# Kernel optimization log

Hardware: AMD Instinct MI355X
Metric: run time of the kernel (lower is better)

Reference implementation:

```python
import jax, jax.numpy as jnp
import numpy as np

B, T, C, HS = 4, 4096, 1024, 128

def setup_inputs() -> dict:
    key = jax.random.key(0)
    kx, kk, kq, kv = jax.random.split(key, 4)
    x = jax.random.normal(kx, (B, T, C), dtype=jnp.float32)
    # torch Linear(n_embd, head_size, bias=False): y = x @ W.T with W [hs, C].
    # We store the transposed form W [C, hs] so y = x @ W (same math).
    s = C ** -0.5  # kaiming-ish scale to keep activations sane
    Wk = jax.random.normal(kk, (C, HS), dtype=jnp.float32) * s
    Wq = jax.random.normal(kq, (C, HS), dtype=jnp.float32) * s
    Wv = jax.random.normal(kv, (C, HS), dtype=jnp.float32) * s
    return {"x": x, "Wk": Wk, "Wq": Wq, "Wv": Wv}

def reference(x, Wk, Wq, Wv):
    # Single causal self-attention head (dropout = identity, eval mode).
    k = jnp.einsum('btc,ch->bth', x, Wk)  # [B,T,hs]
    q = jnp.einsum('btc,ch->bth', x, Wq)
    v = jnp.einsum('btc,ch->bth', x, Wv)
    scale = k.shape[-1] ** -0.5
    wei = jnp.einsum('bqh,bkh->bqk', q, k) * scale  # [B,T,T]
    Tq = x.shape[1]
    causal = jnp.tril(jnp.ones((Tq, Tq), dtype=bool))
    wei = jnp.where(causal, wei, -jnp.inf)
    wei = jax.nn.softmax(wei, axis=-1)
    out = jnp.einsum('bqk,bkh->bqh', wei, v)  # [B,T,hs]
    return out
```

## Files before the change

kernel.cpp:

```cpp
#include <hip/hip_runtime.h>
#include <hip/hip_bf16.h>
#include <math.h>

#define B_  4
#define T_  4096
#define C_  1024
#define HS_ 128

using bf16x8 = __attribute__((ext_vector_type(8))) __bf16;
using bf16x4 = __attribute__((ext_vector_type(4))) __bf16;
using f32x4  = __attribute__((ext_vector_type(4))) float;

#define MFMA(a, b, c) __builtin_amdgcn_mfma_f32_16x16x32_bf16(a, b, c, 0, 0, 0)

typedef __attribute__((address_space(1))) const float gfloat;
typedef __attribute__((address_space(3))) float lfloat;

__device__ inline float fexp2(float x) {
  float r;
  asm volatile("v_exp_f32 %0, %1\n\ts_nop 0" : "=v"(r) : "v"(x));
  return r;
}


__global__ __launch_bounds__(256) void prep_w_kernel(
    const float* __restrict__ Wk, const float* __restrict__ Wq,
    const float* __restrict__ Wv, __bf16* __restrict__ Wf) {
  const int m  = blockIdx.x >> 4;
  const int k0 = (blockIdx.x & 15) * 64;
  const float* W = (m == 0) ? Wq : ((m == 1) ? Wk : Wv);
  const float scale = (m == 0) ? (0.08838834764831845f * 1.4426950408889634f) : 1.0f;
  __shared__ __bf16 tile[128][72];
  const int t = threadIdx.x;
#pragma unroll
  for (int p = 0; p < 8; ++p) {
    int e  = p * 1024 + t * 4;
    int r  = e >> 7;
    int cc = e & 127;
    float4 w = *reinterpret_cast<const float4*>(&W[(size_t)(k0 + r) * HS_ + cc]);
    tile[cc + 0][r] = (__bf16)(w.x * scale);
    tile[cc + 1][r] = (__bf16)(w.y * scale);
    tile[cc + 2][r] = (__bf16)(w.z * scale);
    tile[cc + 3][r] = (__bf16)(w.w * scale);
  }
  __syncthreads();
#pragma unroll
  for (int p = 0; p < 4; ++p) {
    int e  = p * 2048 + t * 8;
    int n  = e >> 6;
    int kk = e & 63;
    bf16x8 v;
#pragma unroll
    for (int jj = 0; jj < 8; ++jj) v[jj] = tile[n][kk + jj];
    int u  = m * 8 + (n >> 4);
    int ts = (k0 + kk) >> 5;
    int g2 = (kk >> 3) & 3;
    *reinterpret_cast<bf16x8*>(
        &Wf[((size_t)(u * 32 + ts) * 64 + g2 * 16 + (n & 15)) * 8]) = v;
  }
}

__device__ inline bf16x8 cvt8p(float4 u, float4 v) {
  bf16x8 r;
  r[0] = (__bf16)u.x; r[1] = (__bf16)u.y; r[2] = (__bf16)u.z; r[3] = (__bf16)u.w;
  r[4] = (__bf16)v.x; r[5] = (__bf16)v.y; r[6] = (__bf16)v.z; r[7] = (__bf16)v.w;
  return r;
}

__global__ __launch_bounds__(512) void proj_kernel(
    const float* __restrict__ x, const __bf16* __restrict__ Wf,
    __bf16* __restrict__ Qf, __bf16* __restrict__ Kf, __bf16* __restrict__ Vf) {
  __shared__ __align__(16) char lds[57344];
  const int tid = threadIdx.x;
  const int wid = tid >> 6;
  const int l   = tid & 63;
  const int c   = l & 15;
  const int g   = l >> 4;
  const int rbase = blockIdx.x * 32;

  f32x4 acc[3][2];
#pragma unroll
  for (int i = 0; i < 3; ++i) { acc[i][0] = 0.f; acc[i][1] = 0.f; }

  const int xrow = (tid & 255) >> 3;
  const int xch  = tid & 7;
  const float* xsrc = x + (size_t)(rbase + xrow) * C_ + ((xch ^ (xrow & 7)) << 2);
  const __bf16* wsrc[3];
  int wdst[3];
#pragma unroll
  for (int i = 0; i < 3; ++i) {
    int id = i * 512 + tid;
    int u  = id >> 6;
    int ln = id & 63;
    wsrc[i] = Wf + (size_t)u * 32 * 512 + ln * 8;
    wdst[i] = 4096 + id * 16;
  }

  auto stage = [&](int t, int bo) {
    if (tid < 256)
      __builtin_amdgcn_global_load_lds((gfloat*)(xsrc + t * 32),
          (lfloat*)(lds + bo + tid * 16), 16, 0, 0);
#pragma unroll
    for (int i = 0; i < 3; ++i)
      __builtin_amdgcn_global_load_lds((gfloat*)(wsrc[i] + t * 512),
          (lfloat*)(lds + bo + wdst[i]), 16, 0, 0);
  };

  int woffs[3];
#pragma unroll
  for (int i = 0; i < 3; ++i)
    woffs[i] = 4096 + (wid * 3 + i) * 1024 + l * 16;
  int xoffs[2][2];
#pragma unroll
  for (int rt = 0; rt < 2; ++rt) {
    int row = rt * 16 + c;
#pragma unroll
    for (int j = 0; j < 2; ++j)
      xoffs[rt][j] = row * 128 + ((((g << 1) | j) ^ (row & 7)) << 4);
  }

  stage(0, 0);
  asm volatile("s_waitcnt vmcnt(0)" ::: "memory");
  __syncthreads();

  for (int t = 0; t < 32; ++t) {
    const int bo = (t & 1) * 28672;
    if (t + 1 < 32) stage(t + 1, bo ^ 28672);

    bf16x8 wf[3];
#pragma unroll
    for (int i = 0; i < 3; ++i)
      wf[i] = *reinterpret_cast<const bf16x8*>(lds + bo + woffs[i]);
#pragma unroll
    for (int rt = 0; rt < 2; ++rt) {
      float4 lo = *reinterpret_cast<const float4*>(lds + bo + xoffs[rt][0]);
      float4 hi = *reinterpret_cast<const float4*>(lds + bo + xoffs[rt][1]);
      bf16x8 a = cvt8p(lo, hi);
#pragma unroll
      for (int i = 0; i < 3; ++i) acc[i][rt] = MFMA(a, wf[i], acc[i][rt]);
    }

    asm volatile("s_waitcnt vmcnt(0)" ::: "memory");
    __syncthreads();
  }

  const size_t tile = blockIdx.x;
#pragma unroll
  for (int i = 0; i < 3; ++i) {
    const int u = wid * 3 + i;
    const int m = u >> 3, nt = u & 7;
    const int gprime = ((nt & 1) << 1) + (c >> 3);
    const int e = c & 7;
    if (m == 0) {
#pragma unroll
      for (int rt = 0; rt < 2; ++rt)
#pragma unroll
        for (int rr = 0; rr < 4; ++rr)
          Qf[(tile * 8 + rt * 4 + (nt >> 1)) * 512 +
             (gprime * 16 + 4 * g + rr) * 8 + e] = (__bf16)acc[i][rt][rr];
    } else if (m == 1) {
#pragma unroll
      for (int rt = 0; rt < 2; ++rt)
#pragma unroll
        for (int rr = 0; rr < 4; ++rr)
          Kf[(tile * 8 + 2 * (nt >> 1) + (g & 1)) * 512 +
             (gprime * 16 + (((2 * rt + (g >> 1)) << 2) | rr)) * 8 + e] =
              (__bf16)acc[i][rt][rr];
    } else {
#pragma unroll
      for (int rt = 0; rt < 2; ++rt) {
        bf16x4 v4;
#pragma unroll
        for (int rr = 0; rr < 4; ++rr) v4[rr] = (__bf16)acc[i][rt][rr];
        *reinterpret_cast<bf16x4*>(
            Vf + (tile * 8 + nt) * 512 +
            ((2 * rt + (g >> 1)) * 16 + c) * 8 + 4 * (g & 1)) = v4;
      }
    }
  }
}

__global__ __launch_bounds__(256, 2) void attn_kernel(
    const __bf16* __restrict__ Qf, const __bf16* __restrict__ Kf,
    const __bf16* __restrict__ Vf, float* __restrict__ out) {
  __shared__ float sm[4][32];
  __shared__ float sl[4][32];
  __shared__ float bufA[32][132];
  __shared__ float bufB[32][132];

  const int tid = threadIdx.x;
  const int wid = tid >> 6;
  const int l   = tid & 63;
  const int c   = l & 15;
  const int g   = l >> 4;
  const int bid = blockIdx.x;
  const int b   = (bid & 7) >> 1;
  const int j   = ((bid >> 3) << 1) | (bid & 1);
  const int qt  = (j < 64) ? (127 - j) : (j - 64);
  const int qb  = qt * 32;

  bf16x8 qf[2][4];
  {
    const __bf16* Qt = Qf + (size_t)(b * 128 + qt) * 4096 + l * 8;
#pragma unroll
    for (int rt = 0; rt < 2; ++rt)
#pragma unroll
      for (int cs = 0; cs < 4; ++cs)
        qf[rt][cs] = *reinterpret_cast<const bf16x8*>(Qt + (rt * 4 + cs) * 512);
  }

  f32x4 acc[2][8];
#pragma unroll
  for (int i = 0; i < 2; ++i)
#pragma unroll
    for (int d = 0; d < 8; ++d) acc[i][d] = 0.f;
  float mrun[2] = {-INFINITY, -INFINITY};
  float lrun[2] = {0.f, 0.f};

  if (wid <= qt) {
    const __bf16* Kb8 = Kf + (size_t)b * 128 * 4096 + l * 8;
    const __bf16* Vb8 = Vf + (size_t)b * 128 * 4096 + l * 8;
    bf16x8 kreg[8];
    auto kload = [&](int kt) {
      const __bf16* kb = Kb8 + (size_t)kt * 4096;
#pragma unroll
      for (int jj = 0; jj < 8; ++jj)
        kreg[jj] = *reinterpret_cast<const bf16x8*>(kb + jj * 512);
    };
    kload(wid);

    for (int kt = wid; kt <= qt; kt += 4) {
      f32x4 s00 = 0.f, s01 = 0.f, s10 = 0.f, s11 = 0.f;
      __builtin_amdgcn_s_setprio(1);
#pragma unroll
      for (int cs = 0; cs < 4; ++cs) {
        s00 = MFMA(kreg[2 * cs], qf[0][cs], s00);
        s01 = MFMA(kreg[2 * cs + 1], qf[0][cs], s01);
        s10 = MFMA(kreg[2 * cs], qf[1][cs], s10);
        s11 = MFMA(kreg[2 * cs + 1], qf[1][cs], s11);
      }
      __builtin_amdgcn_s_setprio(0);

      bf16x8 vf[8];
      {
        const __bf16* vb = Vb8 + (size_t)kt * 4096;
#pragma unroll
        for (int db = 0; db < 8; ++db)
          vf[db] = *reinterpret_cast<const bf16x8*>(vb + db * 512);
      }

      if (kt + 4 <= qt) kload(kt + 4);

      const bool maskt = (kt == qt);
      bf16x8 pb[2];
#pragma unroll
      for (int rt = 0; rt < 2; ++rt) {
        float p[8];
        const f32x4 sa = rt ? s10 : s00;
        const f32x4 sb = rt ? s11 : s01;
#pragma unroll
        for (int rr = 0; rr < 4; ++rr) { p[rr] = sa[rr]; p[4 + rr] = sb[rr]; }
        if (maskt) {
          const int lim = rt * 16 + c;
#pragma unroll
          for (int jj = 0; jj < 8; ++jj)
            if (8 * g + jj > lim) p[jj] = -INFINITY;
        }
        float t0 = fmaxf(fmaxf(p[0], p[1]), p[2]);
        float t1 = fmaxf(fmaxf(p[3], p[4]), p[5]);
        float t2 = fmaxf(fmaxf(p[6], p[7]), t0);
        float tmax = fmaxf(t1, t2);

        if (!__all(tmax <= mrun[rt] + 11.5415603f)) {
          float cmax = fmaxf(tmax, __shfl_xor(tmax, 16));
          cmax = fmaxf(cmax, __shfl_xor(cmax, 32));
          float mnew = fmaxf(mrun[rt], cmax);
          float al   = fexp2(mrun[rt] - mnew);
          mrun[rt] = mnew;
          lrun[rt] *= al;
#pragma unroll
          for (int db = 0; db < 8; ++db) acc[rt][db] *= al;
        }
        const float mc = mrun[rt];
#pragma unroll
        for (int jj = 0; jj < 8; ++jj) p[jj] = fexp2(p[jj] - mc);
        lrun[rt] += ((p[0] + p[1]) + (p[2] + p[3])) + ((p[4] + p[5]) + (p[6] + p[7]));
#pragma unroll
        for (int jj = 0; jj < 8; ++jj) pb[rt][jj] = (__bf16)p[jj];
      }

      __builtin_amdgcn_s_setprio(1);
#pragma unroll
      for (int db = 0; db < 8; ++db) {
        acc[0][db] = MFMA(vf[db], pb[0], acc[0][db]);
        acc[1][db] = MFMA(vf[db], pb[1], acc[1][db]);
      }
      __builtin_amdgcn_s_setprio(0);
    }
  }

#pragma unroll
  for (int rt = 0; rt < 2; ++rt) {
    lrun[rt] += __shfl_xor(lrun[rt], 16);
    lrun[rt] += __shfl_xor(lrun[rt], 32);
  }

  if (g == 0) {
    sm[wid][c] = mrun[0]; sm[wid][16 + c] = mrun[1];
    sl[wid][c] = lrun[0]; sl[wid][16 + c] = lrun[1];
  }
  __syncthreads();

  float linv[2];
#pragma unroll
  for (int rt = 0; rt < 2; ++rt) {
    const int q = rt * 16 + c;
    float ms = fmaxf(fmaxf(sm[0][q], sm[1][q]), fmaxf(sm[2][q], sm[3][q]));
    float ls = fexp2(sm[0][q] - ms) * sl[0][q] + fexp2(sm[1][q] - ms) * sl[1][q]
             + fexp2(sm[2][q] - ms) * sl[2][q] + fexp2(sm[3][q] - ms) * sl[3][q];
    float al = fexp2(mrun[rt] - ms);
#pragma unroll
    for (int db = 0; db < 8; ++db) acc[rt][db] *= al;
    linv[rt] = 1.0f / ls;
  }

  auto store_buf = [&](float(*buf)[132]) {
#pragma unroll
    for (int rt = 0; rt < 2; ++rt)
#pragma unroll
      for (int db = 0; db < 8; ++db)
        *reinterpret_cast<f32x4*>(&buf[rt * 16 + c][db * 16 + 4 * g]) = acc[rt][db];
  };
  auto add_buf = [&](float(*buf)[132]) {
#pragma unroll
    for (int rt = 0; rt < 2; ++rt)
#pragma unroll
      for (int db = 0; db < 8; ++db)
        acc[rt][db] += *reinterpret_cast<const f32x4*>(&buf[rt * 16 + c][db * 16 + 4 * g]);
  };

  if (wid == 2) store_buf(bufA);
  if (wid == 3) store_buf(bufB);
  __syncthreads();
  if (wid == 0) add_buf(bufA);
  if (wid == 1) add_buf(bufB);
  __syncthreads();
  if (wid == 1) store_buf(bufA);
  __syncthreads();
  if (wid == 0) {
    add_buf(bufA);
    float* op = out + ((size_t)b * T_ + qb) * HS_;
#pragma unroll
    for (int rt = 0; rt < 2; ++rt)
#pragma unroll
      for (int db = 0; db < 8; ++db) {
        f32x4 v = acc[rt][db] * linv[rt];
        *reinterpret_cast<f32x4*>(op + (size_t)(rt * 16 + c) * HS_ + db * 16 + 4 * g) = v;
      }
  }
}

extern "C" void kernel_launch(void* const* d_in, const int* in_sizes, int n_in,
                              void* d_out, int out_size, void* d_ws, size_t ws_size,
                              hipStream_t stream) {
  const float* x  = (const float*)d_in[0];
  const float* Wk = (const float*)d_in[1];
  const float* Wq = (const float*)d_in[2];
  const float* Wv = (const float*)d_in[3];
  float* out = (float*)d_out;

  char* ws = (char*)d_ws;
  __bf16* Wf = (__bf16*)ws;
  __bf16* Qf = (__bf16*)(ws + 786432);
  __bf16* Kf = (__bf16*)(ws + 786432 + 4194304);
  __bf16* Vf = (__bf16*)(ws + 786432 + 8388608);

  prep_w_kernel<<<48, 256, 0, stream>>>(Wk, Wq, Wv, Wf);
  proj_kernel<<<512, 512, 0, stream>>>(x, Wf, Qf, Kf, Vf);
  attn_kernel<<<512, 256, 0, stream>>>(Qf, Kf, Vf, out);
}
```

Baseline: 64.77 us.

## Triple-buffer x tiles in projection kernel with deeper prefetch

Splits the projection kernel's staging into separate x and W buffers. x now gets a three-deep LDS ring prefetched two steps ahead, while W stays double-buffered. The x load moves from 16-byte loads on half the threads to 4-byte loads on all threads, and the waitcnt is relaxed to vmcnt(2) so more loads stay in flight. The goal is to hide global latency for x in the K loop, at the cost of more LDS and smaller-granularity loads.

```diff
diff --git a/kernel.cpp b/kernel.cpp
--- a/kernel.cpp
+++ b/kernel.cpp
@@ -70,7 +70,7 @@
 __global__ __launch_bounds__(512) void proj_kernel(
     const float* __restrict__ x, const __bf16* __restrict__ Wf,
     __bf16* __restrict__ Qf, __bf16* __restrict__ Kf, __bf16* __restrict__ Vf) {
-  __shared__ __align__(16) char lds[57344];
+  __shared__ __align__(16) char lds[61440];
   const int tid = threadIdx.x;
   const int wid = tid >> 6;
   const int l   = tid & 63;
@@ -82,9 +82,15 @@
 #pragma unroll
   for (int i = 0; i < 3; ++i) { acc[i][0] = 0.f; acc[i][1] = 0.f; }
 
-  const int xrow = (tid & 255) >> 3;
-  const int xch  = tid & 7;
-  const float* xsrc = x + (size_t)(rbase + xrow) * C_ + ((xch ^ (xrow & 7)) << 2);
+  const float* xsrc[2];
+#pragma unroll
+  for (int op = 0; op < 2; ++op) {
+    int id  = op * 512 + tid;
+    int row = id >> 5;
+    int w   = id & 31;
+    int sf  = ((((w >> 2) ^ (row & 7)) << 2) | (w & 3));
+    xsrc[op] = x + (size_t)(rbase + row) * C_ + sf;
+  }
   const __bf16* wsrc[3];
   int wdst[3];
 #pragma unroll
@@ -93,23 +99,26 @@
     int u  = id >> 6;
     int ln = id & 63;
     wsrc[i] = Wf + (size_t)u * 32 * 512 + ln * 8;
-    wdst[i] = 4096 + id * 16;
-  }
-
-  auto stage = [&](int t, int bo) {
-    if (tid < 256)
-      __builtin_amdgcn_global_load_lds((gfloat*)(xsrc + t * 32),
-          (lfloat*)(lds + bo + tid * 16), 16, 0, 0);
+    wdst[i] = id * 16;
+  }
+
+  auto xstage = [&](int t, int xbo) {
+#pragma unroll
+    for (int op = 0; op < 2; ++op)
+      __builtin_amdgcn_global_load_lds((gfloat*)(xsrc[op] + t * 32),
+          (lfloat*)(lds + xbo + (op * 512 + tid) * 4), 4, 0, 0);
+  };
+  auto wstage = [&](int t, int wbo) {
 #pragma unroll
     for (int i = 0; i < 3; ++i)
       __builtin_amdgcn_global_load_lds((gfloat*)(wsrc[i] + t * 512),
-          (lfloat*)(lds + bo + wdst[i]), 16, 0, 0);
+          (lfloat*)(lds + wbo + wdst[i]), 16, 0, 0);
   };
 
   int woffs[3];
 #pragma unroll
   for (int i = 0; i < 3; ++i)
-    woffs[i] = 4096 + (wid * 3 + i) * 1024 + l * 16;
+    woffs[i] = (wid * 3 + i) * 1024 + l * 16;
   int xoffs[2][2];
 #pragma unroll
   for (int rt = 0; rt < 2; ++rt) {
@@ -119,29 +128,39 @@
       xoffs[rt][j] = row * 128 + ((((g << 1) | j) ^ (row & 7)) << 4);
   }
 
-  stage(0, 0);
-  asm volatile("s_waitcnt vmcnt(0)" ::: "memory");
-  __syncthreads();
-
+  xstage(0, 0);
+  wstage(0, 12288);
+  xstage(1, 4096);
+  asm volatile("s_waitcnt vmcnt(2)" ::: "memory");
+  __syncthreads();
+
+  int xb_cur = 0, xb_nxt = 4096, xb_fut = 8192;
   for (int t = 0; t < 32; ++t) {
-    const int bo = (t & 1) * 28672;
-    if (t + 1 < 32) stage(t + 1, bo ^ 28672);
+    const int wbo = 12288 + (t & 1) * 24576;
+    if (t + 1 < 32) wstage(t + 1, 12288 + ((t + 1) & 1) * 24576);
+    const bool more2 = (t + 2 < 32);
+    if (more2) xstage(t + 2, xb_fut);
 
     bf16x8 wf[3];
 #pragma unroll
     for (int i = 0; i < 3; ++i)
-      wf[i] = *reinterpret_cast<const bf16x8*>(lds + bo + woffs[i]);
+      wf[i] = *reinterpret_cast<const bf16x8*>(lds + wbo + woffs[i]);
 #pragma unroll
     for (int rt = 0; rt < 2; ++rt) {
-      float4 lo = *reinterpret_cast<const float4*>(lds + bo + xoffs[rt][0]);
-      float4 hi = *reinterpret_cast<const float4*>(lds + bo + xoffs[rt][1]);
+      float4 lo = *reinterpret_cast<const float4*>(lds + xb_cur + xoffs[rt][0]);
+      float4 hi = *reinterpret_cast<const float4*>(lds + xb_cur + xoffs[rt][1]);
       bf16x8 a = cvt8p(lo, hi);
 #pragma unroll
       for (int i = 0; i < 3; ++i) acc[i][rt] = MFMA(a, wf[i], acc[i][rt]);
     }
 
-    asm volatile("s_waitcnt vmcnt(0)" ::: "memory");
+    if (more2) {
+      asm volatile("s_waitcnt vmcnt(2)" ::: "memory");
+    } else {
+      asm volatile("s_waitcnt vmcnt(0)" ::: "memory");
+    }
     __syncthreads();
+    int tmp = xb_cur; xb_cur = xb_nxt; xb_nxt = xb_fut; xb_fut = tmp;
   }
 
   const size_t tile = blockIdx.x;
```

Measured after the change: 65.05 us. No clear change (+0.4%).

## Retile projection GEMM to 128-row blocks per Q/K/V matrix

Applied to the files above, without the earlier changes.

The projection kernel now gives each block 128 rows of x and a single output matrix (Q, K or V), with four waves that each compute 32 rows by 128 columns. Before, a block handled 32 rows across all three weights. The new tiling lowers the weight bytes staged per row of x, since each weight tile is reused over 128 rows. The cost is that x is read three times, once per matrix, and the grid shrinks to 384 blocks of 256 threads with more accumulators per thread.

```diff
diff --git a/kernel.cpp b/kernel.cpp
--- a/kernel.cpp
+++ b/kernel.cpp
@@ -67,53 +67,59 @@
   return r;
 }
 
-__global__ __launch_bounds__(512) void proj_kernel(
+__global__ __launch_bounds__(256) void proj_kernel(
     const float* __restrict__ x, const __bf16* __restrict__ Wf,
     __bf16* __restrict__ Qf, __bf16* __restrict__ Kf, __bf16* __restrict__ Vf) {
-  __shared__ __align__(16) char lds[57344];
+  __shared__ __align__(16) char lds[49152];
   const int tid = threadIdx.x;
   const int wid = tid >> 6;
   const int l   = tid & 63;
   const int c   = l & 15;
   const int g   = l >> 4;
-  const int rbase = blockIdx.x * 32;
-
-  f32x4 acc[3][2];
-#pragma unroll
-  for (int i = 0; i < 3; ++i) { acc[i][0] = 0.f; acc[i][1] = 0.f; }
-
-  const int xrow = (tid & 255) >> 3;
-  const int xch  = tid & 7;
-  const float* xsrc = x + (size_t)(rbase + xrow) * C_ + ((xch ^ (xrow & 7)) << 2);
-  const __bf16* wsrc[3];
-  int wdst[3];
-#pragma unroll
-  for (int i = 0; i < 3; ++i) {
-    int id = i * 512 + tid;
-    int u  = id >> 6;
+  const int m       = blockIdx.x % 3;
+  const int rowtile = blockIdx.x / 3;
+  const int rbase   = rowtile * 128;
+
+  f32x4 acc[8][2];
+#pragma unroll
+  for (int i = 0; i < 8; ++i) { acc[i][0] = 0.f; acc[i][1] = 0.f; }
+
+  const float* xsrc[4];
+#pragma unroll
+  for (int op = 0; op < 4; ++op) {
+    int id  = op * 256 + tid;
+    int row = id >> 3;
+    int ch  = id & 7;
+    xsrc[op] = x + (size_t)(rbase + row) * C_ + ((ch ^ (row & 7)) << 2);
+  }
+  const __bf16* wsrc[2];
+#pragma unroll
+  for (int i = 0; i < 2; ++i) {
+    int id = i * 256 + tid;
+    int ul = id >> 6;
     int ln = id & 63;
-    wsrc[i] = Wf + (size_t)u * 32 * 512 + ln * 8;
-    wdst[i] = 4096 + id * 16;
+    wsrc[i] = Wf + (size_t)((m * 8 + ul) * 32) * 512 + ln * 8;
   }
 
   auto stage = [&](int t, int bo) {
-    if (tid < 256)
-      __builtin_amdgcn_global_load_lds((gfloat*)(xsrc + t * 32),
-          (lfloat*)(lds + bo + tid * 16), 16, 0, 0);
-#pragma unroll
-    for (int i = 0; i < 3; ++i)
+#pragma unroll
+    for (int op = 0; op < 4; ++op)
+      __builtin_amdgcn_global_load_lds((gfloat*)(xsrc[op] + t * 32),
+          (lfloat*)(lds + bo + (op * 256 + tid) * 16), 16, 0, 0);
+#pragma unroll
+    for (int i = 0; i < 2; ++i)
       __builtin_amdgcn_global_load_lds((gfloat*)(wsrc[i] + t * 512),
-          (lfloat*)(lds + bo + wdst[i]), 16, 0, 0);
+          (lfloat*)(lds + bo + 16384 + (i * 256 + tid) * 16), 16, 0, 0);
   };
 
-  int woffs[3];
-#pragma unroll
-  for (int i = 0; i < 3; ++i)
-    woffs[i] = 4096 + (wid * 3 + i) * 1024 + l * 16;
+  int woffs[8];
+#pragma unroll
+  for (int nt = 0; nt < 8; ++nt)
+    woffs[nt] = 16384 + nt * 1024 + l * 16;
   int xoffs[2][2];
 #pragma unroll
   for (int rt = 0; rt < 2; ++rt) {
-    int row = rt * 16 + c;
+    int row = wid * 32 + rt * 16 + c;
 #pragma unroll
     for (int j = 0; j < 2; ++j)
       xoffs[rt][j] = row * 128 + ((((g << 1) | j) ^ (row & 7)) << 4);
@@ -124,31 +130,29 @@
   __syncthreads();
 
   for (int t = 0; t < 32; ++t) {
-    const int bo = (t & 1) * 28672;
-    if (t + 1 < 32) stage(t + 1, bo ^ 28672);
-
-    bf16x8 wf[3];
-#pragma unroll
-    for (int i = 0; i < 3; ++i)
-      wf[i] = *reinterpret_cast<const bf16x8*>(lds + bo + woffs[i]);
+    const int bo = (t & 1) * 24576;
+    if (t + 1 < 32) stage(t + 1, bo ^ 24576);
+
+    bf16x8 wf[8];
+#pragma unroll
+    for (int nt = 0; nt < 8; ++nt)
+      wf[nt] = *reinterpret_cast<const bf16x8*>(lds + bo + woffs[nt]);
 #pragma unroll
     for (int rt = 0; rt < 2; ++rt) {
       float4 lo = *reinterpret_cast<const float4*>(lds + bo + xoffs[rt][0]);
       float4 hi = *reinterpret_cast<const float4*>(lds + bo + xoffs[rt][1]);
       bf16x8 a = cvt8p(lo, hi);
 #pragma unroll
-      for (int i = 0; i < 3; ++i) acc[i][rt] = MFMA(a, wf[i], acc[i][rt]);
+      for (int nt = 0; nt < 8; ++nt) acc[nt][rt] = MFMA(a, wf[nt], acc[nt][rt]);
     }
 
     asm volatile("s_waitcnt vmcnt(0)" ::: "memory");
     __syncthreads();
   }
 
-  const size_t tile = blockIdx.x;
-#pragma unroll
-  for (int i = 0; i < 3; ++i) {
-    const int u = wid * 3 + i;
-    const int m = u >> 3, nt = u & 7;
+  const size_t tile = (size_t)rowtile * 4 + wid;
+#pragma unroll
+  for (int nt = 0; nt < 8; ++nt) {
     const int gprime = ((nt & 1) << 1) + (c >> 3);
     const int e = c & 7;
     if (m == 0) {
@@ -157,7 +161,7 @@
 #pragma unroll
         for (int rr = 0; rr < 4; ++rr)
           Qf[(tile * 8 + rt * 4 + (nt >> 1)) * 512 +
-             (gprime * 16 + 4 * g + rr) * 8 + e] = (__bf16)acc[i][rt][rr];
+             (gprime * 16 + 4 * g + rr) * 8 + e] = (__bf16)acc[nt][rt][rr];
     } else if (m == 1) {
 #pragma unroll
       for (int rt = 0; rt < 2; ++rt)
@@ -165,13 +169,13 @@
         for (int rr = 0; rr < 4; ++rr)
           Kf[(tile * 8 + 2 * (nt >> 1) + (g & 1)) * 512 +
              (gprime * 16 + (((2 * rt + (g >> 1)) << 2) | rr)) * 8 + e] =
-              (__bf16)acc[i][rt][rr];
+              (__bf16)acc[nt][rt][rr];
     } else {
 #pragma unroll
       for (int rt = 0; rt < 2; ++rt) {
         bf16x4 v4;
 #pragma unroll
-        for (int rr = 0; rr < 4; ++rr) v4[rr] = (__bf16)acc[i][rt][rr];
+        for (int rr = 0; rr < 4; ++rr) v4[rr] = (__bf16)acc[nt][rt][rr];
         *reinterpret_cast<bf16x4*>(
             Vf + (tile * 8 + nt) * 512 +
             ((2 * rt + (g >> 1)) * 16 + c) * 8 + 4 * (g & 1)) = v4;
@@ -376,6 +380,6 @@
   __bf16* Vf = (__bf16*)(ws + 786432 + 8388608);
 
   prep_w_kernel<<<48, 256, 0, stream>>>(Wk, Wq, Wv, Wf);
-  proj_kernel<<<512, 512, 0, stream>>>(x, Wf, Qf, Kf, Vf);
+  proj_kernel<<<384, 256, 0, stream>>>(x, Wf, Qf, Kf, Vf);
   attn_kernel<<<512, 256, 0, stream>>>(Qf, Kf, Vf, out);
 }
```

Measured after the change: 72.93 us, median of 2. 1.13x slower.
